# Kernel tuning notes

Measured on AMD Instinct MI355X. Metric: run time of the kernel, lower is better.

Reference implementation:

```python
import jax, jax.numpy as jnp
import numpy as np

# Canonical Mamba hyperparams (mamba_ssm defaults for d_model=128)
D_MODEL = 128
D_INNER = 2 * D_MODEL          # expand = 2
D_STATE = 16
D_CONV = 4
DT_RANK = (D_MODEL + 15) // 16  # ceil(d_model/16) = 8
B, N, T = 16, 256, 64
EPS = 1e-5


def setup_inputs() -> dict:
    key = jax.random.key(0)
    ks = jax.random.split(key, 10)
    sc = 0.02
    x = jax.random.normal(ks[0], (B, N, D_MODEL, T), jnp.float32)
    gamma = jnp.ones((D_MODEL,), jnp.float32)
    beta = jnp.zeros((D_MODEL,), jnp.float32)
    W_in = jax.random.normal(ks[1], (D_MODEL, 2 * D_INNER), jnp.float32) * sc
    conv_w = jax.random.normal(ks[2], (D_INNER, D_CONV), jnp.float32) * sc
    conv_b = jnp.zeros((D_INNER,), jnp.float32)
    W_x = jax.random.normal(ks[3], (D_INNER, DT_RANK + 2 * D_STATE), jnp.float32) * sc
    W_dt = jax.random.normal(ks[4], (DT_RANK, D_INNER), jnp.float32) * sc
    b_dt = jax.random.normal(ks[5], (D_INNER,), jnp.float32) * sc
    # S4D-real init: A_log = log(1..d_state), broadcast over channels
    A_log = jnp.log(jnp.broadcast_to(
        jnp.arange(1, D_STATE + 1, dtype=jnp.float32), (D_INNER, D_STATE)))
    Dskip = jnp.ones((D_INNER,), jnp.float32)
    W_out = jax.random.normal(ks[6], (D_INNER, D_MODEL), jnp.float32) * sc
    return dict(x=x, gamma=gamma, beta=beta, W_in=W_in, conv_w=conv_w,
                conv_b=conv_b, W_x=W_x, W_dt=W_dt, b_dt=b_dt,
                A_log=A_log, Dskip=Dskip, W_out=W_out)


def _forward(x, gamma, beta, W_in, conv_w, conv_b, W_x, W_dt, b_dt,
             A_log, Dskip, W_out):
    Bb, Nn, Fd, Tt = x.shape
    # (B,N,F,T) -> (B*N, T, F)
    x_in = x.transpose(0, 1, 3, 2).reshape(Bb * Nn, Tt, Fd)

    # LayerNorm over feature dim
    mu = x_in.mean(-1, keepdims=True)
    var = jnp.mean((x_in - mu) ** 2, axis=-1, keepdims=True)
    u = (x_in - mu) * jax.lax.rsqrt(var + EPS) * gamma + beta

    # Mamba: input projection -> (x, z)
    xz = u @ W_in                                   # (BN,T,2*dI)
    xc, z = jnp.split(xz, 2, axis=-1)

    # Depthwise causal conv1d over time (kernel D_CONV) + SiLU
    xp = jnp.pad(xc, ((0, 0), (D_CONV - 1, 0), (0, 0)))
    xconv = sum(xp[:, k:k + Tt, :] * conv_w[:, k] for k in range(D_CONV)) + conv_b
    xact = jax.nn.silu(xconv)                       # (BN,T,dI)

    # Input-dependent SSM parameters
    dbl = xact @ W_x                                # (BN,T,dt_rank+2*dS)
    dt = dbl[..., :DT_RANK]
    Bm = dbl[..., DT_RANK:DT_RANK + D_STATE]        # (BN,T,dS)
    Cm = dbl[..., DT_RANK + D_STATE:]               # (BN,T,dS)
    delta = jax.nn.softplus(dt @ W_dt + b_dt)       # (BN,T,dI)
    A = -jnp.exp(A_log)                             # (dI,dS)

    # Selective scan over time
    def step(h, inp):
        d, b, c, xt = inp                            # (BN,dI) (BN,dS) (BN,dS) (BN,dI)
        dA = jnp.exp(d[:, :, None] * A)              # (BN,dI,dS)
        h = dA * h + (d * xt)[:, :, None] * b[:, None, :]
        y = jnp.einsum('bis,bs->bi', h, c)
        return h, y

    h0 = jnp.zeros((Bb * Nn, D_INNER, D_STATE), x.dtype)
    seq = (delta.transpose(1, 0, 2), Bm.transpose(1, 0, 2),
           Cm.transpose(1, 0, 2), xact.transpose(1, 0, 2))
    _, ys = jax.lax.scan(step, h0, seq)             # (T,BN,dI)
    y = ys.transpose(1, 0, 2) + xact * Dskip
    y = y * jax.nn.silu(z)
    out = y @ W_out                                 # (BN,T,d_model)

    # Residual (dropout is identity in eval/reference), reshape back
    x_out = out + x_in
    return x_out.reshape(Bb, Nn, Tt, Fd).transpose(0, 1, 3, 2)


def reference(x, gamma, beta, W_in, conv_w, conv_b, W_x, W_dt, b_dt,
              A_log, Dskip, W_out):
    return _forward(x, gamma, beta, W_in, conv_w, conv_b, W_x, W_dt, b_dt,
                    A_log, Dskip, W_out)
```

## Files before the change

### kernel.cpp

```cpp
#include <hip/hip_runtime.h>
#include <stdint.h>

typedef unsigned short ushort_t;
typedef __attribute__((ext_vector_type(8))) short bf16x8;
typedef __attribute__((ext_vector_type(4))) float f32x4;

#define P_CONVW 0
#define P_CONVB 1024
#define P_BDT   1280
#define P_A     1536
#define P_DSKIP 5632
#define P_GAMMA 5888
#define P_BETA  6016
#define P_WDT   6144
#define P_TOT   8192

#define OFFB_WINT   0
#define OFFB_WXT    131072
#define OFFB_WOUTT  163840
#define OFFB_PF     229376
#define OFFB_DYN    262144

__device__ __forceinline__ float b2f(ushort_t u) {
    return __uint_as_float(((unsigned int)u) << 16);
}
__device__ __forceinline__ ushort_t f2b(float f) {
    unsigned int x = __float_as_uint(f);
    return (ushort_t)((x + 0x7fffu + ((x >> 16) & 1u)) >> 16);
}
__device__ __forceinline__ bool is_f32_mode(const void* gamma) {
    return ((const unsigned int*)gamma)[0] == 0x3F800000u;
}
__device__ __forceinline__ float ld_any(const void* p, int idx, bool f32m) {
    return f32m ? ((const float*)p)[idx] : b2f(((const ushort_t*)p)[idx]);
}
__device__ __forceinline__ float silu_f(float v) {
    return v * __builtin_amdgcn_rcpf(1.0f + __expf(-v));
}

__global__ __launch_bounds__(256) void prep_kernel(
    const void* __restrict__ gamma, const void* __restrict__ beta,
    const void* __restrict__ W_in,  const void* __restrict__ conv_w,
    const void* __restrict__ conv_b,const void* __restrict__ W_x,
    const void* __restrict__ W_dt,  const void* __restrict__ b_dt,
    const void* __restrict__ A_log, const void* __restrict__ Dskip,
    const void* __restrict__ W_out, char* __restrict__ wsb)
{
    const bool f32m = is_f32_mode(gamma);
    ushort_t* WinT  = (ushort_t*)(wsb + OFFB_WINT);
    ushort_t* WxT   = (ushort_t*)(wsb + OFFB_WXT);
    ushort_t* WoutT = (ushort_t*)(wsb + OFFB_WOUTT);
    float*    pf    = (float*)(wsb + OFFB_PF);
    int idx = blockIdx.x * 256 + threadIdx.x;

    if (idx < 65536) {
        int n = idx >> 7, k = idx & 127;
        WinT[idx] = f2b(ld_any(W_in, k * 512 + n, f32m));
    }
    if (idx < 16384) {
        int n = idx >> 8, k = idx & 255;
        WxT[idx] = (n < 40) ? f2b(ld_any(W_x, k * 40 + n, f32m)) : (ushort_t)0;
    }
    if (idx < 32768) {
        int n = idx >> 8, k = idx & 255;
        WoutT[idx] = f2b(ld_any(W_out, k * 128 + n, f32m));
    }
    if (idx < 1024) pf[P_CONVW + idx] = ld_any(conv_w, idx, f32m);
    if (idx < 4096) pf[P_A + idx]     = -__expf(ld_any(A_log, idx, f32m));
    if (idx < 2048) pf[P_WDT + idx]   = ld_any(W_dt, idx, f32m);
    if (idx < 256) {
        pf[P_CONVB + idx] = ld_any(conv_b, idx, f32m);
        pf[P_BDT + idx]   = ld_any(b_dt, idx, f32m);
        pf[P_DSKIP + idx] = ld_any(Dskip, idx, f32m);
    }
    if (idx < 128) {
        pf[P_GAMMA + idx] = ld_any(gamma, idx, f32m);
        pf[P_BETA + idx]  = ld_any(beta, idx, f32m);
    }
}

__global__ __launch_bounds__(256) void k_ln(
    const void* __restrict__ x_v, const void* __restrict__ gamma_v,
    const float* __restrict__ pf, ushort_t* __restrict__ u_out, int seq_base)
{
    __shared__ __align__(16) float uT[128 * 72];
    __shared__ float red1[256], red2[256];
    __shared__ float mu_s[64], rs_s[64];

    const int tid = threadIdx.x;
    const int sloc = blockIdx.x;
    const bool f32m = is_f32_mode(gamma_v);
    const size_t seq_off = (size_t)(seq_base + sloc) * (128 * 64);

    {
        int f = tid >> 1, th = tid & 1;
        float* dst = uT + f * 72 + th * 32;
        if (!f32m) {
            const uint4* src = (const uint4*)((const ushort_t*)x_v + seq_off + f * 64 + th * 32);
            #pragma unroll
            for (int i = 0; i < 4; ++i) {
                uint4 q = src[i];
                *(float4*)(dst + i * 8) = make_float4(
                    __uint_as_float(q.x << 16), __uint_as_float(q.x & 0xffff0000u),
                    __uint_as_float(q.y << 16), __uint_as_float(q.y & 0xffff0000u));
                *(float4*)(dst + i * 8 + 4) = make_float4(
                    __uint_as_float(q.z << 16), __uint_as_float(q.z & 0xffff0000u),
                    __uint_as_float(q.w << 16), __uint_as_float(q.w & 0xffff0000u));
            }
        } else {
            const float4* src = (const float4*)((const float*)x_v + seq_off + f * 64 + th * 32);
            #pragma unroll
            for (int i = 0; i < 8; ++i) *(float4*)(dst + i * 4) = src[i];
        }
    }
    __syncthreads();
    {
        int q = tid >> 6, t = tid & 63;
        float su = 0.f, sq = 0.f;
        #pragma unroll 8
        for (int kk = 0; kk < 32; ++kk) {
            float v = uT[(q * 32 + kk) * 72 + t];
            su += v; sq += v * v;
        }
        red1[tid] = su; red2[tid] = sq;
    }
    __syncthreads();
    if (tid < 64) {
        float su = red1[tid] + red1[64 + tid] + red1[128 + tid] + red1[192 + tid];
        float sq = red2[tid] + red2[64 + tid] + red2[128 + tid] + red2[192 + tid];
        float mu = su * (1.0f / 128.0f);
        float var = sq * (1.0f / 128.0f) - mu * mu;
        mu_s[tid] = mu;
        rs_s[tid] = rsqrtf(var + 1e-5f);
    }
    __syncthreads();
    {
        int t = tid & 63, dq = tid >> 6;
        float mu = mu_s[t], rs = rs_s[t];
        unsigned int pk[16];
        #pragma unroll
        for (int j = 0; j < 16; ++j) {
            int d0 = dq * 32 + 2 * j;
            float v0 = (uT[d0 * 72 + t] - mu) * rs * pf[P_GAMMA + d0] + pf[P_BETA + d0];
            float v1 = (uT[(d0 + 1) * 72 + t] - mu) * rs * pf[P_GAMMA + d0 + 1] + pf[P_BETA + d0 + 1];
            pk[j] = (unsigned int)f2b(v0) | ((unsigned int)f2b(v1) << 16);
        }
        uint4* dst = (uint4*)(u_out + (size_t)(sloc * 64 + t) * 128 + dq * 32);
        dst[0] = make_uint4(pk[0], pk[1], pk[2], pk[3]);
        dst[1] = make_uint4(pk[4], pk[5], pk[6], pk[7]);
        dst[2] = make_uint4(pk[8], pk[9], pk[10], pk[11]);
        dst[3] = make_uint4(pk[12], pk[13], pk[14], pk[15]);
    }
}

__global__ __launch_bounds__(512) void k_gemm1(
    const ushort_t* __restrict__ u, const ushort_t* __restrict__ WinT,
    ushort_t* __restrict__ xz, int nrows)
{
    __shared__ __align__(16) ushort_t Afr[16384];
    const int tid = threadIdx.x;
    const int m0 = blockIdx.x * 128;

    #pragma unroll
    for (int i = 0; i < 4; ++i) {
        int g = tid * 4 + i;
        int R = g >> 4, cc = g & 15;
        uint4 val = make_uint4(0u, 0u, 0u, 0u);
        int row = m0 + R;
        if (row < nrows) val = *(const uint4*)(u + (size_t)row * 128 + cc * 8);
        int kstep = cc >> 2, q = cc & 3, mf = R >> 4, r = R & 15;
        *(uint4*)(Afr + (((kstep * 8 + mf) * 64) + q * 16 + r) * 8) = val;
    }
    __syncthreads();

    const int lane = tid & 63, w = tid >> 6;
    const int wm = w & 1, wn = w >> 1;
    const int r = lane & 15, q = lane >> 4;

    #pragma unroll 1
    for (int nt = 0; nt < 4; ++nt) {
        f32x4 acc[4][2];
        #pragma unroll
        for (int i = 0; i < 4; ++i)
            #pragma unroll
            for (int nf = 0; nf < 2; ++nf) acc[i][nf] = (f32x4)(0.0f);

        #pragma unroll
        for (int ks = 0; ks < 4; ++ks) {
            bf16x8 a[4], b[2];
            #pragma unroll
            for (int i = 0; i < 4; ++i)
                a[i] = *(const bf16x8*)(Afr + ((ks * 8 + wm * 4 + i) * 64 + lane) * 8);
            #pragma unroll
            for (int nf = 0; nf < 2; ++nf) {
                int n = nt * 128 + wn * 32 + nf * 16 + r;
                b[nf] = *(const bf16x8*)(WinT + n * 128 + ks * 32 + q * 8);
            }
            #pragma unroll
            for (int i = 0; i < 4; ++i)
                #pragma unroll
                for (int nf = 0; nf < 2; ++nf)
                    acc[i][nf] = __builtin_amdgcn_mfma_f32_16x16x32_bf16(a[i], b[nf], acc[i][nf], 0, 0, 0);
        }
        #pragma unroll
        for (int i = 0; i < 4; ++i)
            #pragma unroll
            for (int nf = 0; nf < 2; ++nf)
                #pragma unroll
                for (int rg = 0; rg < 4; ++rg) {
                    int m = m0 + wm * 64 + i * 16 + q * 4 + rg;
                    if (m < nrows) {
                        int n = nt * 128 + wn * 32 + nf * 16 + r;
                        xz[(size_t)m * 512 + n] = f2b(acc[i][nf][rg]);
                    }
                }
    }
}

__global__ __launch_bounds__(256, 4) void k_fuse(
    const void* __restrict__ x_v, const void* __restrict__ gamma_v,
    const ushort_t* __restrict__ xz, const float* __restrict__ pf,
    const ushort_t* __restrict__ WxT, const ushort_t* __restrict__ WoutT,
    void* __restrict__ out_v, int seq_base)
{
    __shared__ __align__(16) char smem[40448];
    ushort_t* xact_s = (ushort_t*)smem;
    float*    dt_s   = (float*)(smem + 33792);
    ushort_t* BC_s   = (ushort_t*)(smem + 35840);

    const int tid = threadIdx.x;
    const int sloc = blockIdx.x;
    const int sglob = seq_base + sloc;
    const bool f32m = is_f32_mode(gamma_v);
    const int lane = tid & 63, w = tid >> 6;
    const int r = lane & 15, q = lane >> 4;

    {
        const int c = tid;
        float cw0 = pf[P_CONVW + c * 4 + 0], cw1 = pf[P_CONVW + c * 4 + 1];
        float cw2 = pf[P_CONVW + c * 4 + 2], cw3 = pf[P_CONVW + c * 4 + 3];
        float cb  = pf[P_CONVB + c];
        float w0 = 0.f, w1 = 0.f, w2 = 0.f;
        const ushort_t* xc = xz + (size_t)sloc * 64 * 512 + c;
        #pragma unroll 4
        for (int t = 0; t < 64; ++t) {
            float xv = b2f(xc[t * 512]);
            float v = cb + w0 * cw0 + w1 * cw1 + w2 * cw2 + xv * cw3;
            xact_s[t * 264 + c] = f2b(silu_f(v));
            w0 = w1; w1 = w2; w2 = xv;
        }
    }
    __syncthreads();

    {
        f32x4 acc2[4];
        #pragma unroll
        for (int i = 0; i < 4; ++i) acc2[i] = (f32x4)(0.0f);
        #pragma unroll 1
        for (int ks = 0; ks < 8; ++ks) {
            bf16x8 b = *(const bf16x8*)(WxT + (w * 16 + r) * 256 + ks * 32 + q * 8);
            #pragma unroll
            for (int i = 0; i < 4; ++i) {
                bf16x8 a = *(const bf16x8*)(xact_s + (i * 16 + r) * 264 + ks * 32 + q * 8);
                acc2[i] = __builtin_amdgcn_mfma_f32_16x16x32_bf16(a, b, acc2[i], 0, 0, 0);
            }
        }
        int col = w * 16 + r;
        #pragma unroll
        for (int i = 0; i < 4; ++i)
            #pragma unroll
            for (int rg = 0; rg < 4; ++rg) {
                int trow = i * 16 + q * 4 + rg;
                float v = acc2[i][rg];
                if (col < 8)       dt_s[trow * 8 + col] = v;
                else if (col < 40) BC_s[trow * 36 + (col - 8)] = f2b(v);
            }
    }
    __syncthreads();

    {
        const int i = tid;
        float wdt[8];
        #pragma unroll
        for (int rr = 0; rr < 8; ++rr) wdt[rr] = pf[P_WDT + rr * 256 + i];
        const float bdt = pf[P_BDT + i];
        const float dsk = pf[P_DSKIP + i];

        bool structured = true;
        #pragma unroll
        for (int ss = 0; ss < 16; ++ss) {
            float av = pf[P_A + i * 16 + ss];
            structured = structured && (fabsf(av + (float)(ss + 1)) <= 1e-3f * (float)(ss + 1));
        }

        float h[16];
        #pragma unroll
        for (int ss = 0; ss < 16; ++ss) h[ss] = 0.f;
        const ushort_t* zc = xz + (size_t)sloc * 64 * 512 + 256 + i;

        auto dt_arg = [&](int t) -> float {
            const float* dr = dt_s + t * 8;
            float4 d0 = *(const float4*)dr;
            float4 d1 = *(const float4*)(dr + 4);
            float arg = bdt;
            arg = fmaf(d0.x, wdt[0], arg); arg = fmaf(d0.y, wdt[1], arg);
            arg = fmaf(d0.z, wdt[2], arg); arg = fmaf(d0.w, wdt[3], arg);
            arg = fmaf(d1.x, wdt[4], arg); arg = fmaf(d1.y, wdt[5], arg);
            arg = fmaf(d1.z, wdt[6], arg); arg = fmaf(d1.w, wdt[7], arg);
            return arg;
        };

        if (structured) {
            auto scan_step = [&](int t, float delv, float e1v, float xtv,
                                 ushort_t zv, const unsigned int* pk) {
                float Bv[16], Cv[16];
                #pragma unroll
                for (int jj = 0; jj < 8; ++jj) {
                    unsigned int v = pk[jj];
                    Bv[2 * jj]     = __uint_as_float(v << 16);
                    Bv[2 * jj + 1] = __uint_as_float(v & 0xffff0000u);
                }
                #pragma unroll
                for (int jj = 0; jj < 8; ++jj) {
                    unsigned int v = pk[8 + jj];
                    Cv[2 * jj]     = __uint_as_float(v << 16);
                    Cv[2 * jj + 1] = __uint_as_float(v & 0xffff0000u);
                }
                float dx = delv * xtv;
                float dA = e1v;
                float yp[4] = {0.f, 0.f, 0.f, 0.f};
                #pragma unroll
                for (int ss = 0; ss < 16; ++ss) {
                    h[ss] = fmaf(dA, h[ss], dx * Bv[ss]);
                    yp[ss & 3] = fmaf(h[ss], Cv[ss], yp[ss & 3]);
                    dA *= e1v;
                }
                float y = (yp[0] + yp[1]) + (yp[2] + yp[3]);
                float yg = fmaf(xtv, dsk, y) * silu_f(b2f(zv));
                xact_s[t * 264 + i] = f2b(yg);
            };

            float e1_c, del_c;
            {
                float arg = dt_arg(0);
                float p = __expf(arg);
                float opp = 1.0f + p;
                e1_c = __builtin_amdgcn_rcpf(opp);
                del_c = __logf(opp);
            }
            unsigned int pk_c[16];
            {
                const uint2* bq = (const uint2*)(BC_s);
                #pragma unroll
                for (int jj = 0; jj < 8; ++jj) {
                    uint2 vv = bq[jj];
                    pk_c[2 * jj] = vv.x; pk_c[2 * jj + 1] = vv.y;
                }
            }
            float xt_c = b2f(xact_s[i]);
            ushort_t z_c = zc[0];
            ushort_t z_n = zc[512];

            #pragma unroll 1
            for (int t = 0; t < 63; ++t) {
                float arg = dt_arg(t + 1);
                float p = __expf(arg);
                float opp = 1.0f + p;
                float e1_n = __builtin_amdgcn_rcpf(opp);
                float del_n = __logf(opp);
                unsigned int pk_n[16];
                {
                    const uint2* bq = (const uint2*)(BC_s + (t + 1) * 36);
                    #pragma unroll
                    for (int jj = 0; jj < 8; ++jj) {
                        uint2 vv = bq[jj];
                        pk_n[2 * jj] = vv.x; pk_n[2 * jj + 1] = vv.y;
                    }
                }
                float xt_n = b2f(xact_s[(t + 1) * 264 + i]);
                int tz = (t + 2 <= 63) ? (t + 2) : 63;
                ushort_t z_n2 = zc[(size_t)tz * 512];

                scan_step(t, del_c, e1_c, xt_c, z_c, pk_c);

                e1_c = e1_n; del_c = del_n; xt_c = xt_n;
                z_c = z_n; z_n = z_n2;
                #pragma unroll
                for (int jj = 0; jj < 16; ++jj) pk_c[jj] = pk_n[jj];
            }
            scan_step(63, del_c, e1_c, xt_c, z_c, pk_c);
        } else {
            float Av[16];
            #pragma unroll
            for (int ss = 0; ss < 16; ++ss) Av[ss] = pf[P_A + i * 16 + ss];
            #pragma unroll 1
            for (int t = 0; t < 64; ++t) {
                float arg = dt_arg(t);
                float delta = __logf(1.0f + __expf(arg));
                unsigned int pk[16];
                const uint2* bq = (const uint2*)(BC_s + t * 36);
                #pragma unroll
                for (int jj = 0; jj < 8; ++jj) {
                    uint2 vv = bq[jj];
                    pk[2 * jj] = vv.x; pk[2 * jj + 1] = vv.y;
                }
                float Bv[16], Cv[16];
                #pragma unroll
                for (int jj = 0; jj < 8; ++jj) {
                    unsigned int v = pk[jj];
                    Bv[2 * jj]     = __uint_as_float(v << 16);
                    Bv[2 * jj + 1] = __uint_as_float(v & 0xffff0000u);
                    unsigned int vc = pk[8 + jj];
                    Cv[2 * jj]     = __uint_as_float(vc << 16);
                    Cv[2 * jj + 1] = __uint_as_float(vc & 0xffff0000u);
                }
                float xt = b2f(xact_s[t * 264 + i]);
                float zf = b2f(zc[t * 512]);
                float dx = delta * xt;
                float y = 0.f;
                #pragma unroll
                for (int ss = 0; ss < 16; ++ss) {
                    float dA = __expf(delta * Av[ss]);
                    h[ss] = fmaf(dA, h[ss], dx * Bv[ss]);
                    y = fmaf(h[ss], Cv[ss], y);
                }
                float yg = fmaf(xt, dsk, y) * silu_f(zf);
                xact_s[t * 264 + i] = f2b(yg);
            }
        }
    }
    __syncthreads();

    {
        f32x4 acc3[4][2];
        #pragma unroll
        for (int i = 0; i < 4; ++i)
            #pragma unroll
            for (int nf = 0; nf < 2; ++nf) acc3[i][nf] = (f32x4)(0.0f);
        #pragma unroll 1
        for (int ks = 0; ks < 8; ++ks) {
            bf16x8 a[4], b[2];
            #pragma unroll
            for (int i = 0; i < 4; ++i)
                a[i] = *(const bf16x8*)(xact_s + (i * 16 + r) * 264 + ks * 32 + q * 8);
            #pragma unroll
            for (int nf = 0; nf < 2; ++nf)
                b[nf] = *(const bf16x8*)(WoutT + (w * 32 + nf * 16 + r) * 256 + ks * 32 + q * 8);
            #pragma unroll
            for (int i = 0; i < 4; ++i)
                #pragma unroll
                for (int nf = 0; nf < 2; ++nf)
                    acc3[i][nf] = __builtin_amdgcn_mfma_f32_16x16x32_bf16(a[i], b[nf], acc3[i][nf], 0, 0, 0);
        }
        if (!f32m) {
            #pragma unroll
            for (int i = 0; i < 4; ++i)
                #pragma unroll
                for (int nf = 0; nf < 2; ++nf) {
                    int d = w * 32 + nf * 16 + r;
                    int tb = i * 16 + q * 4;
                    size_t off = (size_t)sglob * 8192 + (size_t)d * 64 + tb;
                    uint2 xv = *(const uint2*)((const ushort_t*)x_v + off);
                    float x0 = __uint_as_float(xv.x << 16);
                    float x1 = __uint_as_float(xv.x & 0xffff0000u);
                    float x2 = __uint_as_float(xv.y << 16);
                    float x3 = __uint_as_float(xv.y & 0xffff0000u);
                    uint2 res;
                    res.x = (unsigned int)f2b(acc3[i][nf][0] + x0) |
                            ((unsigned int)f2b(acc3[i][nf][1] + x1) << 16);
                    res.y = (unsigned int)f2b(acc3[i][nf][2] + x2) |
                            ((unsigned int)f2b(acc3[i][nf][3] + x3) << 16);
                    *(uint2*)((ushort_t*)out_v + off) = res;
                }
        } else {
            #pragma unroll
            for (int i = 0; i < 4; ++i)
                #pragma unroll
                for (int nf = 0; nf < 2; ++nf) {
                    int d = w * 32 + nf * 16 + r;
                    int tb = i * 16 + q * 4;
                    size_t off = (size_t)sglob * 8192 + (size_t)d * 64 + tb;
                    float4 xv = *(const float4*)((const float*)x_v + off);
                    float4 res = make_float4(acc3[i][nf][0] + xv.x,
                                             acc3[i][nf][1] + xv.y,
                                             acc3[i][nf][2] + xv.z,
                                             acc3[i][nf][3] + xv.w);
                    *(float4*)((float*)out_v + off) = res;
                }
        }
    }
}

extern "C" void kernel_launch(void* const* d_in, const int* in_sizes, int n_in,
                              void* d_out, int out_size, void* d_ws, size_t ws_size,
                              hipStream_t stream)
{
    const void* x      = d_in[0];
    const void* gamma  = d_in[1];
    const void* beta   = d_in[2];
    const void* W_in   = d_in[3];
    const void* conv_w = d_in[4];
    const void* conv_b = d_in[5];
    const void* W_x    = d_in[6];
    const void* W_dt   = d_in[7];
    const void* b_dt   = d_in[8];
    const void* A_log  = d_in[9];
    const void* Dskip  = d_in[10];
    const void* W_out  = d_in[11];

    char* wsb = (char*)d_ws;
    long long avail = (long long)ws_size - OFFB_DYN;
    long long S = avail > 0 ? avail / 81920 : 1;
    if (S > 4096) S = 4096;
    if (S < 1) S = 1;

    ushort_t* WinT  = (ushort_t*)(wsb + OFFB_WINT);
    ushort_t* WxT   = (ushort_t*)(wsb + OFFB_WXT);
    ushort_t* WoutT = (ushort_t*)(wsb + OFFB_WOUTT);
    float*    pf    = (float*)(wsb + OFFB_PF);
    ushort_t* u_buf = (ushort_t*)(wsb + OFFB_DYN);
    ushort_t* xz_buf= (ushort_t*)(wsb + OFFB_DYN + S * 16384);

    prep_kernel<<<dim3(256), dim3(256), 0, stream>>>(
        gamma, beta, W_in, conv_w, conv_b, W_x, W_dt, b_dt, A_log, Dskip, W_out, wsb);

    for (int base = 0; base < 4096; base += (int)S) {
        int cnt = 4096 - base < (int)S ? 4096 - base : (int)S;
        k_ln<<<dim3(cnt), dim3(256), 0, stream>>>(x, gamma, pf, u_buf, base);
        k_gemm1<<<dim3((cnt + 1) / 2), dim3(512), 0, stream>>>(u_buf, WinT, xz_buf, cnt * 64);
        k_fuse<<<dim3(cnt), dim3(256), 0, stream>>>(x, gamma, xz_buf, pf, WxT, WoutT, d_out, base);
    }
}
```

Before: 691.5 us.

## Fuse LayerNorm into input GEMM, transpose xz layout, pack scan math

LayerNorm and the input projection GEMM now run in one kernel, so the bf16 u buffer no longer makes a round trip through global memory and one launch per chunk is removed. The x half of xz is stored time-contiguous per channel so the conv can read it with vectorized loads, and z moves to its own region with a 256 stride. The structured selective scan is rewritten with packed v_pk_fma/v_pk_mul f32 ops, processes two timesteps per iteration with prefetch, and packs both outputs with one bf16 convert. In exchange the fused kernel does less GEMM work per block (64 rows per 256-thread block) and makes an extra pass over WinT per block, and the BC row stride and shared-memory size change.

```diff
diff --git a/kernel.cpp b/kernel.cpp
--- a/kernel.cpp
+++ b/kernel.cpp
@@ -4,6 +4,7 @@
 typedef unsigned short ushort_t;
 typedef __attribute__((ext_vector_type(8))) short bf16x8;
 typedef __attribute__((ext_vector_type(4))) float f32x4;
+typedef __attribute__((ext_vector_type(2))) float f32x2;
 
 #define P_CONVW 0
 #define P_CONVB 1024
@@ -36,6 +37,15 @@
 }
 __device__ __forceinline__ float silu_f(float v) {
     return v * __builtin_amdgcn_rcpf(1.0f + __expf(-v));
+}
+__device__ __forceinline__ f32x2 pk_fma(f32x2 a, f32x2 b, f32x2 c) {
+    f32x2 d; asm("v_pk_fma_f32 %0, %1, %2, %3" : "=v"(d) : "v"(a), "v"(b), "v"(c)); return d;
+}
+__device__ __forceinline__ f32x2 pk_mul(f32x2 a, f32x2 b) {
+    f32x2 d; asm("v_pk_mul_f32 %0, %1, %2" : "=v"(d) : "v"(a), "v"(b)); return d;
+}
+__device__ __forceinline__ f32x2 pk_add(f32x2 a, f32x2 b) {
+    f32x2 d; asm("v_pk_add_f32 %0, %1, %2" : "=v"(d) : "v"(a), "v"(b)); return d;
 }
 
 __global__ __launch_bounds__(256) void prep_kernel(
@@ -79,33 +89,35 @@
     }
 }
 
-__global__ __launch_bounds__(256) void k_ln(
+__global__ __launch_bounds__(256, 3) void k_lngemm1(
     const void* __restrict__ x_v, const void* __restrict__ gamma_v,
-    const float* __restrict__ pf, ushort_t* __restrict__ u_out, int seq_base)
+    const float* __restrict__ pf, const ushort_t* __restrict__ WinT,
+    ushort_t* __restrict__ xz, int seq_base)
 {
-    __shared__ __align__(16) float uT[128 * 72];
+    __shared__ __align__(16) float uT[128 * 68];
+    __shared__ __align__(16) ushort_t Afr[8192];
     __shared__ float red1[256], red2[256];
     __shared__ float mu_s[64], rs_s[64];
 
     const int tid = threadIdx.x;
     const int sloc = blockIdx.x;
     const bool f32m = is_f32_mode(gamma_v);
-    const size_t seq_off = (size_t)(seq_base + sloc) * (128 * 64);
+    const size_t seq_off = (size_t)(seq_base + sloc) * 8192;
 
     {
         int f = tid >> 1, th = tid & 1;
-        float* dst = uT + f * 72 + th * 32;
+        float* dst = uT + f * 68 + th * 32;
         if (!f32m) {
             const uint4* src = (const uint4*)((const ushort_t*)x_v + seq_off + f * 64 + th * 32);
             #pragma unroll
             for (int i = 0; i < 4; ++i) {
-                uint4 q = src[i];
+                uint4 qd = src[i];
                 *(float4*)(dst + i * 8) = make_float4(
-                    __uint_as_float(q.x << 16), __uint_as_float(q.x & 0xffff0000u),
-                    __uint_as_float(q.y << 16), __uint_as_float(q.y & 0xffff0000u));
+                    __uint_as_float(qd.x << 16), __uint_as_float(qd.x & 0xffff0000u),
+                    __uint_as_float(qd.y << 16), __uint_as_float(qd.y & 0xffff0000u));
                 *(float4*)(dst + i * 8 + 4) = make_float4(
-                    __uint_as_float(q.z << 16), __uint_as_float(q.z & 0xffff0000u),
-                    __uint_as_float(q.w << 16), __uint_as_float(q.w & 0xffff0000u));
+                    __uint_as_float(qd.z << 16), __uint_as_float(qd.z & 0xffff0000u),
+                    __uint_as_float(qd.w << 16), __uint_as_float(qd.w & 0xffff0000u));
             }
         } else {
             const float4* src = (const float4*)((const float*)x_v + seq_off + f * 64 + th * 32);
@@ -115,11 +127,11 @@
     }
     __syncthreads();
     {
-        int q = tid >> 6, t = tid & 63;
+        int qq = tid >> 6, t = tid & 63;
         float su = 0.f, sq = 0.f;
         #pragma unroll 8
         for (int kk = 0; kk < 32; ++kk) {
-            float v = uT[(q * 32 + kk) * 72 + t];
+            float v = uT[(qq * 32 + kk) * 68 + t];
             su += v; sq += v * v;
         }
         red1[tid] = su; red2[tid] = sq;
@@ -137,83 +149,81 @@
     {
         int t = tid & 63, dq = tid >> 6;
         float mu = mu_s[t], rs = rs_s[t];
-        unsigned int pk[16];
-        #pragma unroll
-        for (int j = 0; j < 16; ++j) {
-            int d0 = dq * 32 + 2 * j;
-            float v0 = (uT[d0 * 72 + t] - mu) * rs * pf[P_GAMMA + d0] + pf[P_BETA + d0];
-            float v1 = (uT[(d0 + 1) * 72 + t] - mu) * rs * pf[P_GAMMA + d0 + 1] + pf[P_BETA + d0 + 1];
-            pk[j] = (unsigned int)f2b(v0) | ((unsigned int)f2b(v1) << 16);
-        }
-        uint4* dst = (uint4*)(u_out + (size_t)(sloc * 64 + t) * 128 + dq * 32);
-        dst[0] = make_uint4(pk[0], pk[1], pk[2], pk[3]);
-        dst[1] = make_uint4(pk[4], pk[5], pk[6], pk[7]);
-        dst[2] = make_uint4(pk[8], pk[9], pk[10], pk[11]);
-        dst[3] = make_uint4(pk[12], pk[13], pk[14], pk[15]);
-    }
-}
-
-__global__ __launch_bounds__(512) void k_gemm1(
-    const ushort_t* __restrict__ u, const ushort_t* __restrict__ WinT,
-    ushort_t* __restrict__ xz, int nrows)
-{
-    __shared__ __align__(16) ushort_t Afr[16384];
-    const int tid = threadIdx.x;
-    const int m0 = blockIdx.x * 128;
-
-    #pragma unroll
-    for (int i = 0; i < 4; ++i) {
-        int g = tid * 4 + i;
-        int R = g >> 4, cc = g & 15;
-        uint4 val = make_uint4(0u, 0u, 0u, 0u);
-        int row = m0 + R;
-        if (row < nrows) val = *(const uint4*)(u + (size_t)row * 128 + cc * 8);
-        int kstep = cc >> 2, q = cc & 3, mf = R >> 4, r = R & 15;
-        *(uint4*)(Afr + (((kstep * 8 + mf) * 64) + q * 16 + r) * 8) = val;
-    }
-    __syncthreads();
-
-    const int lane = tid & 63, w = tid >> 6;
-    const int wm = w & 1, wn = w >> 1;
-    const int r = lane & 15, q = lane >> 4;
-
-    #pragma unroll 1
-    for (int nt = 0; nt < 4; ++nt) {
-        f32x4 acc[4][2];
-        #pragma unroll
-        for (int i = 0; i < 4; ++i)
-            #pragma unroll
-            for (int nf = 0; nf < 2; ++nf) acc[i][nf] = (f32x4)(0.0f);
-
-        #pragma unroll
-        for (int ks = 0; ks < 4; ++ks) {
-            bf16x8 a[4], b[2];
+        int mf = t >> 4, r = t & 15;
+        #pragma unroll
+        for (int k = 0; k < 4; ++k) {
+            unsigned int pk4[4];
+            #pragma unroll
+            for (int e = 0; e < 4; ++e) {
+                int d0 = dq * 32 + k * 8 + 2 * e;
+                float v0 = (uT[d0 * 68 + t] - mu) * rs * pf[P_GAMMA + d0] + pf[P_BETA + d0];
+                float v1 = (uT[(d0 + 1) * 68 + t] - mu) * rs * pf[P_GAMMA + d0 + 1] + pf[P_BETA + d0 + 1];
+                pk4[e] = (unsigned int)f2b(v0) | ((unsigned int)f2b(v1) << 16);
+            }
+            *(uint4*)(Afr + ((dq * 4 + mf) * 64 + k * 16 + r) * 8) =
+                make_uint4(pk4[0], pk4[1], pk4[2], pk4[3]);
+        }
+    }
+    __syncthreads();
+
+    {
+        const int lane = tid & 63, w = tid >> 6;
+        const int r = lane & 15, q = lane >> 4;
+        const size_t xzbase = (size_t)sloc * 32768;
+
+        #pragma unroll 1
+        for (int nh = 0; nh < 2; ++nh) {
+            f32x4 acc[4][4];
             #pragma unroll
             for (int i = 0; i < 4; ++i)
-                a[i] = *(const bf16x8*)(Afr + ((ks * 8 + wm * 4 + i) * 64 + lane) * 8);
-            #pragma unroll
-            for (int nf = 0; nf < 2; ++nf) {
-                int n = nt * 128 + wn * 32 + nf * 16 + r;
-                b[nf] = *(const bf16x8*)(WinT + n * 128 + ks * 32 + q * 8);
-            }
-            #pragma unroll
-            for (int i = 0; i < 4; ++i)
-                #pragma unroll
-                for (int nf = 0; nf < 2; ++nf)
-                    acc[i][nf] = __builtin_amdgcn_mfma_f32_16x16x32_bf16(a[i], b[nf], acc[i][nf], 0, 0, 0);
-        }
-        #pragma unroll
-        for (int i = 0; i < 4; ++i)
-            #pragma unroll
-            for (int nf = 0; nf < 2; ++nf)
-                #pragma unroll
-                for (int rg = 0; rg < 4; ++rg) {
-                    int m = m0 + wm * 64 + i * 16 + q * 4 + rg;
-                    if (m < nrows) {
-                        int n = nt * 128 + wn * 32 + nf * 16 + r;
-                        xz[(size_t)m * 512 + n] = f2b(acc[i][nf][rg]);
+                #pragma unroll
+                for (int nf = 0; nf < 4; ++nf) acc[i][nf] = (f32x4)(0.0f);
+
+            #pragma unroll
+            for (int ks = 0; ks < 4; ++ks) {
+                bf16x8 a[4], b[4];
+                #pragma unroll
+                for (int i = 0; i < 4; ++i)
+                    a[i] = *(const bf16x8*)(Afr + ((ks * 4 + i) * 64 + lane) * 8);
+                #pragma unroll
+                for (int nf = 0; nf < 4; ++nf) {
+                    int n = w * 128 + nh * 64 + nf * 16 + r;
+                    b[nf] = *(const bf16x8*)(WinT + (size_t)n * 128 + ks * 32 + q * 8);
+                }
+                #pragma unroll
+                for (int i = 0; i < 4; ++i)
+                    #pragma unroll
+                    for (int nf = 0; nf < 4; ++nf)
+                        acc[i][nf] = __builtin_amdgcn_mfma_f32_16x16x32_bf16(a[i], b[nf], acc[i][nf], 0, 0, 0);
+            }
+            if (w < 2) {
+                #pragma unroll
+                for (int i = 0; i < 4; ++i)
+                    #pragma unroll
+                    for (int nf = 0; nf < 4; ++nf) {
+                        int n = w * 128 + nh * 64 + nf * 16 + r;
+                        int tb = i * 16 + q * 4;
+                        uint2 res;
+                        res.x = (unsigned int)f2b(acc[i][nf][0]) |
+                                ((unsigned int)f2b(acc[i][nf][1]) << 16);
+                        res.y = (unsigned int)f2b(acc[i][nf][2]) |
+                                ((unsigned int)f2b(acc[i][nf][3]) << 16);
+                        *(uint2*)(xz + xzbase + (size_t)n * 64 + tb) = res;
                     }
-                }
+            } else {
+                #pragma unroll
+                for (int i = 0; i < 4; ++i)
+                    #pragma unroll
+                    for (int nf = 0; nf < 4; ++nf) {
+                        int n = w * 128 + nh * 64 + nf * 16 + r;
+                        #pragma unroll
+                        for (int rg = 0; rg < 4; ++rg) {
+                            int trow = i * 16 + q * 4 + rg;
+                            xz[xzbase + 16384 + (size_t)trow * 256 + (n - 256)] = f2b(acc[i][nf][rg]);
+                        }
+                    }
+            }
+        }
     }
 }
 
@@ -223,7 +233,7 @@
     const ushort_t* __restrict__ WxT, const ushort_t* __restrict__ WoutT,
     void* __restrict__ out_v, int seq_base)
 {
-    __shared__ __align__(16) char smem[40448];
+    __shared__ __align__(16) char smem[40960];
     ushort_t* xact_s = (ushort_t*)smem;
     float*    dt_s   = (float*)(smem + 33792);
     ushort_t* BC_s   = (ushort_t*)(smem + 35840);
@@ -234,6 +244,7 @@
     const bool f32m = is_f32_mode(gamma_v);
     const int lane = tid & 63, w = tid >> 6;
     const int r = lane & 15, q = lane >> 4;
+    const size_t xzbase = (size_t)sloc * 32768;
 
     {
         const int c = tid;
@@ -241,13 +252,24 @@
         float cw2 = pf[P_CONVW + c * 4 + 2], cw3 = pf[P_CONVW + c * 4 + 3];
         float cb  = pf[P_CONVB + c];
         float w0 = 0.f, w1 = 0.f, w2 = 0.f;
-        const ushort_t* xc = xz + (size_t)sloc * 64 * 512 + c;
-        #pragma unroll 4
-        for (int t = 0; t < 64; ++t) {
-            float xv = b2f(xc[t * 512]);
-            float v = cb + w0 * cw0 + w1 * cw1 + w2 * cw2 + xv * cw3;
-            xact_s[t * 264 + c] = f2b(silu_f(v));
-            w0 = w1; w1 = w2; w2 = xv;
+        const uint4* xq = (const uint4*)(xz + xzbase + (size_t)c * 64);
+        #pragma unroll
+        for (int ch = 0; ch < 4; ++ch) {
+            uint4 a0 = xq[2 * ch], a1 = xq[2 * ch + 1];
+            unsigned int wds[8] = {a0.x, a0.y, a0.z, a0.w, a1.x, a1.y, a1.z, a1.w};
+            #pragma unroll
+            for (int jj = 0; jj < 8; ++jj) {
+                unsigned int v = wds[jj];
+                int t = ch * 16 + jj * 2;
+                float xv0 = __uint_as_float(v << 16);
+                float o0 = cb + w0 * cw0 + w1 * cw1 + w2 * cw2 + xv0 * cw3;
+                xact_s[t * 264 + c] = f2b(silu_f(o0));
+                w0 = w1; w1 = w2; w2 = xv0;
+                float xv1 = __uint_as_float(v & 0xffff0000u);
+                float o1 = cb + w0 * cw0 + w1 * cw1 + w2 * cw2 + xv1 * cw3;
+                xact_s[(t + 1) * 264 + c] = f2b(silu_f(o1));
+                w0 = w1; w1 = w2; w2 = xv1;
+            }
         }
     }
     __syncthreads();
@@ -273,7 +295,7 @@
                 int trow = i * 16 + q * 4 + rg;
                 float v = acc2[i][rg];
                 if (col < 8)       dt_s[trow * 8 + col] = v;
-                else if (col < 40) BC_s[trow * 36 + (col - 8)] = f2b(v);
+                else if (col < 40) BC_s[trow * 40 + (col - 8)] = f2b(v);
             }
     }
     __syncthreads();
@@ -293,10 +315,7 @@
             structured = structured && (fabsf(av + (float)(ss + 1)) <= 1e-3f * (float)(ss + 1));
         }
 
-        float h[16];
-        #pragma unroll
-        for (int ss = 0; ss < 16; ++ss) h[ss] = 0.f;
-        const ushort_t* zc = xz + (size_t)sloc * 64 * 512 + 256 + i;
+        const ushort_t* zc = xz + xzbase + 16384 + i;
 
         auto dt_arg = [&](int t) -> float {
             const float* dr = dt_s + t * 8;
@@ -311,94 +330,89 @@
         };
 
         if (structured) {
-            auto scan_step = [&](int t, float delv, float e1v, float xtv,
-                                 ushort_t zv, const unsigned int* pk) {
-                float Bv[16], Cv[16];
-                #pragma unroll
-                for (int jj = 0; jj < 8; ++jj) {
-                    unsigned int v = pk[jj];
-                    Bv[2 * jj]     = __uint_as_float(v << 16);
-                    Bv[2 * jj + 1] = __uint_as_float(v & 0xffff0000u);
-                }
-                #pragma unroll
-                for (int jj = 0; jj < 8; ++jj) {
-                    unsigned int v = pk[8 + jj];
-                    Cv[2 * jj]     = __uint_as_float(v << 16);
-                    Cv[2 * jj + 1] = __uint_as_float(v & 0xffff0000u);
-                }
-                float dx = delv * xtv;
-                float dA = e1v;
-                float yp[4] = {0.f, 0.f, 0.f, 0.f};
-                #pragma unroll
-                for (int ss = 0; ss < 16; ++ss) {
-                    h[ss] = fmaf(dA, h[ss], dx * Bv[ss]);
-                    yp[ss & 3] = fmaf(h[ss], Cv[ss], yp[ss & 3]);
-                    dA *= e1v;
-                }
-                float y = (yp[0] + yp[1]) + (yp[2] + yp[3]);
-                float yg = fmaf(xtv, dsk, y) * silu_f(b2f(zv));
-                xact_s[t * 264 + i] = f2b(yg);
-            };
-
-            float e1_c, del_c;
-            {
-                float arg = dt_arg(0);
+            f32x2 h2[8];
+            #pragma unroll
+            for (int p = 0; p < 8; ++p) h2[p] = (f32x2){0.f, 0.f};
+
+            f32x2 dAA[8], dAB[8];
+            float dxA, xtA, sgA, dxB, xtB, sgB;
+
+            auto PF = [&](int t, f32x2* dA, float& dx, float& xt, float& sg, ushort_t zv) {
+                float arg = dt_arg(t);
                 float p = __expf(arg);
                 float opp = 1.0f + p;
-                e1_c = __builtin_amdgcn_rcpf(opp);
-                del_c = __logf(opp);
-            }
-            unsigned int pk_c[16];
-            {
-                const uint2* bq = (const uint2*)(BC_s);
-                #pragma unroll
-                for (int jj = 0; jj < 8; ++jj) {
-                    uint2 vv = bq[jj];
-                    pk_c[2 * jj] = vv.x; pk_c[2 * jj + 1] = vv.y;
-                }
-            }
-            float xt_c = b2f(xact_s[i]);
+                float e1 = __builtin_amdgcn_rcpf(opp);
+                float del = __logf(opp);
+                float e2 = e1 * e1, e4 = e2 * e2, e8 = e4 * e4;
+                f32x2 m2 = {e2, e2}, m4 = {e4, e4}, m8 = {e8, e8};
+                dA[0] = (f32x2){e1, e2};
+                dA[1] = pk_mul(dA[0], m2);
+                dA[2] = pk_mul(dA[0], m4);
+                dA[3] = pk_mul(dA[1], m4);
+                dA[4] = pk_mul(dA[0], m8);
+                dA[5] = pk_mul(dA[1], m8);
+                dA[6] = pk_mul(dA[2], m8);
+                dA[7] = pk_mul(dA[3], m8);
+                xt = b2f(xact_s[t * 264 + i]);
+                dx = del * xt;
+                sg = silu_f(b2f(zv));
+            };
+
+            auto STEP = [&](int t, const f32x2* dA, float dx, float xt, float sg) -> float {
+                const uint4* bq = (const uint4*)(BC_s + t * 40);
+                uint4 b0 = bq[0], b1 = bq[1], b2v = bq[2], b3 = bq[3];
+                unsigned int pw[16] = {b0.x, b0.y, b0.z, b0.w, b1.x, b1.y, b1.z, b1.w,
+                                       b2v.x, b2v.y, b2v.z, b2v.w, b3.x, b3.y, b3.z, b3.w};
+                f32x2 dx2 = {dx, dx};
+                f32x2 ya = {0.f, 0.f}, yb = {0.f, 0.f};
+                #pragma unroll
+                for (int p = 0; p < 8; ++p) {
+                    unsigned int v = pw[p];
+                    f32x2 B2 = {__uint_as_float(v << 16), __uint_as_float(v & 0xffff0000u)};
+                    unsigned int vc = pw[8 + p];
+                    f32x2 C2 = {__uint_as_float(vc << 16), __uint_as_float(vc & 0xffff0000u)};
+                    f32x2 bx = pk_mul(B2, dx2);
+                    h2[p] = pk_fma(dA[p], h2[p], bx);
+                    if (p & 1) yb = pk_fma(h2[p], C2, yb);
+                    else       ya = pk_fma(h2[p], C2, ya);
+                }
+                f32x2 ys = pk_add(ya, yb);
+                float y = ys[0] + ys[1];
+                return fmaf(xt, dsk, y) * sg;
+            };
+
             ushort_t z_c = zc[0];
-            ushort_t z_n = zc[512];
+            ushort_t z_n = zc[256];
+            PF(0, dAA, dxA, xtA, sgA, z_c);
+            z_c = z_n; z_n = zc[2 * 256];
 
             #pragma unroll 1
-            for (int t = 0; t < 63; ++t) {
-                float arg = dt_arg(t + 1);
-                float p = __expf(arg);
-                float opp = 1.0f + p;
-                float e1_n = __builtin_amdgcn_rcpf(opp);
-                float del_n = __logf(opp);
-                unsigned int pk_n[16];
-                {
-                    const uint2* bq = (const uint2*)(BC_s + (t + 1) * 36);
-                    #pragma unroll
-                    for (int jj = 0; jj < 8; ++jj) {
-                        uint2 vv = bq[jj];
-                        pk_n[2 * jj] = vv.x; pk_n[2 * jj + 1] = vv.y;
-                    }
-                }
-                float xt_n = b2f(xact_s[(t + 1) * 264 + i]);
-                int tz = (t + 2 <= 63) ? (t + 2) : 63;
-                ushort_t z_n2 = zc[(size_t)tz * 512];
-
-                scan_step(t, del_c, e1_c, xt_c, z_c, pk_c);
-
-                e1_c = e1_n; del_c = del_n; xt_c = xt_n;
-                z_c = z_n; z_n = z_n2;
-                #pragma unroll
-                for (int jj = 0; jj < 16; ++jj) pk_c[jj] = pk_n[jj];
-            }
-            scan_step(63, del_c, e1_c, xt_c, z_c, pk_c);
+            for (int t = 0; t < 64; t += 2) {
+                PF(t + 1, dAB, dxB, xtB, sgB, z_c);
+                { int tz = (t + 3 > 63) ? 63 : t + 3; z_c = z_n; z_n = zc[tz * 256]; }
+                float ygA = STEP(t, dAA, dxA, xtA, sgA);
+                int t2 = (t + 2 > 63) ? 63 : t + 2;
+                PF(t2, dAA, dxA, xtA, sgA, z_c);
+                { int tz = (t + 4 > 63) ? 63 : t + 4; z_c = z_n; z_n = zc[tz * 256]; }
+                float ygB = STEP(t + 1, dAB, dxB, xtB, sgB);
+                unsigned int pkk;
+                asm("v_cvt_pk_bf16_f32 %0, %1, %2" : "=v"(pkk) : "v"(ygA), "v"(ygB));
+                xact_s[t * 264 + i] = (ushort_t)(pkk & 0xffffu);
+                xact_s[(t + 1) * 264 + i] = (ushort_t)(pkk >> 16);
+            }
         } else {
             float Av[16];
             #pragma unroll
             for (int ss = 0; ss < 16; ++ss) Av[ss] = pf[P_A + i * 16 + ss];
+            float h[16];
+            #pragma unroll
+            for (int ss = 0; ss < 16; ++ss) h[ss] = 0.f;
             #pragma unroll 1
             for (int t = 0; t < 64; ++t) {
                 float arg = dt_arg(t);
                 float delta = __logf(1.0f + __expf(arg));
                 unsigned int pk[16];
-                const uint2* bq = (const uint2*)(BC_s + t * 36);
+                const uint2* bq = (const uint2*)(BC_s + t * 40);
                 #pragma unroll
                 for (int jj = 0; jj < 8; ++jj) {
                     uint2 vv = bq[jj];
@@ -415,7 +429,7 @@
                     Cv[2 * jj + 1] = __uint_as_float(vc & 0xffff0000u);
                 }
                 float xt = b2f(xact_s[t * 264 + i]);
-                float zf = b2f(zc[t * 512]);
+                float zf = b2f(zc[t * 256]);
                 float dx = delta * xt;
                 float y = 0.f;
                 #pragma unroll
@@ -510,7 +524,7 @@
 
     char* wsb = (char*)d_ws;
     long long avail = (long long)ws_size - OFFB_DYN;
-    long long S = avail > 0 ? avail / 81920 : 1;
+    long long S = avail > 0 ? avail / 65536 : 1;
     if (S > 4096) S = 4096;
     if (S < 1) S = 1;
 
@@ -518,16 +532,14 @@
     ushort_t* WxT   = (ushort_t*)(wsb + OFFB_WXT);
     ushort_t* WoutT = (ushort_t*)(wsb + OFFB_WOUTT);
     float*    pf    = (float*)(wsb + OFFB_PF);
-    ushort_t* u_buf = (ushort_t*)(wsb + OFFB_DYN);
-    ushort_t* xz_buf= (ushort_t*)(wsb + OFFB_DYN + S * 16384);
+    ushort_t* xz_buf= (ushort_t*)(wsb + OFFB_DYN);
 
     prep_kernel<<<dim3(256), dim3(256), 0, stream>>>(
         gamma, beta, W_in, conv_w, conv_b, W_x, W_dt, b_dt, A_log, Dskip, W_out, wsb);
 
     for (int base = 0; base < 4096; base += (int)S) {
         int cnt = 4096 - base < (int)S ? 4096 - base : (int)S;
-        k_ln<<<dim3(cnt), dim3(256), 0, stream>>>(x, gamma, pf, u_buf, base);
-        k_gemm1<<<dim3((cnt + 1) / 2), dim3(512), 0, stream>>>(u_buf, WinT, xz_buf, cnt * 64);
+        k_lngemm1<<<dim3(cnt), dim3(256), 0, stream>>>(x, gamma, pf, WinT, xz_buf, base);
         k_fuse<<<dim3(cnt), dim3(256), 0, stream>>>(x, gamma, xz_buf, pf, WxT, WoutT, d_out, base);
     }
 }
```

New measurement: 709.7 us. +2.6%, slower.
